# Kernel tuning notes

Hardware: AMD Instinct MI355X
Metric: run time of the kernel (lower is better)

## Reference

```python
import jax, jax.numpy as jnp
import numpy as np
from jax import lax

B, T, CIN, H, W = 2, 6, 1, 256, 256
COUT = 64
L = 13
H2, W2 = H // 2, W // 2


def conv2d(x, w, b, stride=1, pad=0):
    y = lax.conv_general_dilated(x, w, (stride, stride), [(pad, pad), (pad, pad)],
                                 dimension_numbers=('NCHW', 'OIHW', 'NCHW'))
    return y + b[None, :, None, None]


def leaky(x):
    return jnp.where(x >= 0, x, 0.2 * x)


def bilinear_sample(img, sx, sy):
    # img [B,C,H,W]; sx,sy [B,L,H,W] pixel coords; zero padding (grid_sample align_corners=True)
    Bc, C, Hh, Ww = img.shape
    x0 = jnp.floor(sx); y0 = jnp.floor(sy)
    x1 = x0 + 1.0; y1 = y0 + 1.0
    wx1 = sx - x0; wx0 = 1.0 - wx1
    wy1 = sy - y0; wy0 = 1.0 - wy1
    img_flat = img.reshape(Bc, C, Hh * Ww)

    def gather(xi, yi):
        valid = (xi >= 0) & (xi <= Ww - 1) & (yi >= 0) & (yi <= Hh - 1)
        xc = jnp.clip(xi, 0, Ww - 1).astype(jnp.int32)
        yc = jnp.clip(yi, 0, Hh - 1).astype(jnp.int32)
        idx = (yc * Ww + xc).reshape(Bc, 1, -1)
        g = jnp.take_along_axis(img_flat, idx, axis=2).reshape(Bc, C, *xi.shape[1:])
        return g * valid[:, None].astype(img.dtype)  # [B,C,L,H,W]

    return (gather(x0, y0) * (wx0 * wy0)[:, None]
            + gather(x1, y0) * (wx1 * wy0)[:, None]
            + gather(x0, y1) * (wx0 * wy1)[:, None]
            + gather(x1, y1) * (wx1 * wy1)[:, None])


def setup_inputs() -> dict:
    key = jax.random.key(0)
    ks = jax.random.split(key, 14)
    s = 0.05
    return {
        'x': jax.random.normal(ks[0], (B, T, CIN, H, W), jnp.float32),
        'w_stem': jax.random.normal(ks[1], (COUT * T, CIN * T, 3, 3), jnp.float32) * s,
        'b_stem': jnp.zeros((COUT * T,), jnp.float32),
        'w_i2h': jax.random.normal(ks[2], (3 * COUT, COUT, 3, 3), jnp.float32) * s,
        'b_i2h': jnp.zeros((3 * COUT,), jnp.float32),
        'w_i2f': jax.random.normal(ks[3], (32, COUT, 5, 5), jnp.float32) * s,
        'b_i2f': jnp.zeros((32,), jnp.float32),
        'w_h2f': jax.random.normal(ks[4], (32, COUT, 5, 5), jnp.float32) * s,
        'b_h2f': jnp.zeros((32,), jnp.float32),
        'w_flow': jax.random.normal(ks[5], (L * 2, 32, 5, 5), jnp.float32) * s,
        'b_flow': jnp.zeros((L * 2,), jnp.float32),
        'w_ret': jax.random.normal(ks[6], (3 * COUT, L * COUT, 1, 1), jnp.float32) * s,
        'b_ret': jnp.zeros((3 * COUT,), jnp.float32),
    }


def reference(x, w_stem, b_stem, w_i2h, b_i2h, w_i2f, b_i2f, w_h2f, b_h2f,
              w_flow, b_flow, w_ret, b_ret):
    Bq, Tq, Cq, Hq, Wq = x.shape
    h2, w2 = Hq // 2, Wq // 2
    # stem: fold T into channels, strided conv + leaky relu
    xs = x.reshape(Bq, Tq * Cq, Hq, Wq)
    ys = leaky(conv2d(xs, w_stem, b_stem, stride=2, pad=1))
    ys = ys.reshape(Bq, Tq, COUT, h2, w2)
    seq = jnp.transpose(ys, (1, 0, 2, 3, 4))  # [T,B,C,h,w]

    gy, gx = jnp.meshgrid(jnp.arange(h2, dtype=jnp.float32),
                          jnp.arange(w2, dtype=jnp.float32), indexing='ij')

    def step(hprev, xt):
        i2h = conv2d(xt, w_i2h, b_i2h, pad=1)  # [B,3C,h,w]
        f1 = leaky(conv2d(xt, w_i2f, b_i2f, pad=2) + conv2d(hprev, w_h2f, b_h2f, pad=2))
        flows = conv2d(f1, w_flow, b_flow, pad=2).reshape(Bq, L, 2, h2, w2)
        u, v = flows[:, :, 0], flows[:, :, 1]
        # wrap(h, -flow): sample at grid - flow
        sx = gx[None, None] - u
        sy = gy[None, None] - v
        warped = bilinear_sample(hprev, sx, sy)  # [B,C,L,h,w]
        warped = jnp.transpose(warped, (0, 2, 1, 3, 4)).reshape(Bq, L * COUT, h2, w2)
        h2h = conv2d(warped, w_ret, b_ret)  # 1x1 conv
        ir, iu, im = jnp.split(i2h, 3, axis=1)
        hr, hu, hm = jnp.split(h2h, 3, axis=1)
        r = jax.nn.sigmoid(ir + hr)
        z = jax.nn.sigmoid(iu + hu)
        m = leaky(im + r * hm)
        hnext = z * hprev + (1.0 - z) * m
        return hnext, hnext

    h0 = jnp.zeros((Bq, COUT, h2, w2), x.dtype)
    _, outs = lax.scan(step, h0, seq)  # [T,B,C,h,w]
    return jnp.transpose(outs, (1, 0, 2, 3, 4))
```

## Files before the change

### kernel.cpp

```cpp
#include <hip/hip_runtime.h>
#include <cstddef>

#define NPIX 16384
#define T_ 6

typedef __attribute__((ext_vector_type(8))) short bf16x8;
typedef __attribute__((ext_vector_type(4))) float f32x4;

__device__ __forceinline__ float leakyf(float x){ return x >= 0.f ? x : 0.2f*x; }
__device__ __forceinline__ float sigmf(float x){ return 1.f/(1.f+__expf(-x)); }
__device__ __forceinline__ short f2bf(float f){
    unsigned u = __float_as_uint(f);
    u += 0x7fffu + ((u>>16)&1u);
    return (short)(u>>16);
}
__device__ __forceinline__ float bf2f(short s){
    return __uint_as_float(((unsigned)(unsigned short)s)<<16);
}
__device__ __forceinline__ f32x4 MFMA(bf16x8 a, bf16x8 b, f32x4 c){
    return __builtin_amdgcn_mfma_f32_16x16x32_bf16(a, b, c, 0, 0, 0);
}

__global__ __launch_bounds__(256) void prep_w(const float* __restrict__ wi2h,
        const float* __restrict__ wf1i, const float* __restrict__ wf1h,
        const float* __restrict__ wfl, const float* __restrict__ wrt,
        const float* __restrict__ wst, short* __restrict__ dst){
    int idx = blockIdx.x*256 + threadIdx.x;
    float v;
    if(idx < 110592){
        int kk = idx/12288, r = idx%12288, oc = r>>6, ic = r&63;
        v = wi2h[((size_t)(oc*64+ic))*9 + kk];
    } else if(idx < 212992){
        int j = idx-110592; int tap = j>>11, r = j&2047, oc = r>>6, ic = r&63;
        int inp = tap/25, q = tap%25;
        const float* s = inp ? wf1h : wf1i;
        v = s[((size_t)(oc*64+ic))*25 + q];
    } else if(idx < 238592){
        int j = idx-212992; int q = j>>10, r = j&1023, oc = r>>5, ic = r&31;
        v = (oc < 26) ? wfl[((size_t)(oc*32+ic))*25 + q] : 0.f;
    } else if(idx < 398336){
        int j = idx-238592; int s_ = j/6144, r = j%6144, oc = r>>5, c = r&31;
        v = wrt[(size_t)oc*832 + s_*32 + c];
    } else {
        int j = idx-398336; int oc = j>>6, k = j&63;
        if(k < 54){ int ic = k/9, kk = k%9; v = wst[((size_t)(oc*6+ic))*9 + kk]; }
        else v = 0.f;
    }
    dst[idx] = f2bf(v);
}

__global__ __launch_bounds__(256) void stem_mfma(const float* __restrict__ x,
        const short* __restrict__ wS, const float* __restrict__ bias, short* __restrict__ ys_cl){
    __shared__ float xh[6*17*18];
    int bx = blockIdx.x;
    int ohalf = bx & 1, tile = (bx>>1) & 255, b = bx>>9;
    int ty0 = (tile>>4)*8, tx0 = (tile&15)*8;
    int tid = threadIdx.x, wid = tid>>6, lane = tid&63, lr = lane&15, lg = lane>>4;
    int iy0 = ty0*2-1, ix0 = tx0*2-1;
    for(int i=tid; i<1734; i+=256){
        int ic = i/289, r = i%289, hy = r/17, hx = r%17;
        int iy = iy0+hy, ix = ix0+hx;
        float v = 0.f;
        if((unsigned)iy<256u && (unsigned)ix<256u) v = x[((size_t)b*6+ic)*65536 + iy*256 + ix];
        xh[(ic*17+hy)*18+hx] = v;
    }
    __syncthreads();
    int pxl = wid*16 + lr;
    int ry = (pxl>>3)*2, rx = (pxl&7)*2;
    bf16x8 a[2];
    #pragma unroll
    for(int cg=0; cg<2; ++cg){
        #pragma unroll
        for(int e=0; e<8; ++e){
            int k = cg*32 + lg*8 + e;
            float v = 0.f;
            if(k < 54){
                int ic = k/9, t9 = k%9, ky = t9/3, kx = t9%3;
                v = xh[(ic*17 + ry+ky)*18 + rx+kx];
            }
            a[cg][e] = f2bf(v);
        }
    }
    short* yb = ys_cl + (size_t)b*NPIX*384;
    #pragma unroll
    for(int nj=0; nj<12; ++nj){
        int oc = (ohalf*12 + nj)*16 + lr;
        f32x4 acc = {};
        #pragma unroll
        for(int cg=0; cg<2; ++cg){
            bf16x8 bb = *(const bf16x8*)&wS[(size_t)oc*64 + cg*32 + lg*8];
            acc = MFMA(a[cg], bb, acc);
        }
        float bvs = bias[oc];
        #pragma unroll
        for(int r=0; r<4; ++r){
            int pxr = wid*16 + lg*4 + r;
            int pix = (ty0 + (pxr>>3))*128 + tx0 + (pxr&7);
            yb[(size_t)pix*384 + oc] = f2bf(leakyf(acc[r]+bvs));
        }
    }
}

__global__ __launch_bounds__(512) void ih_if_mfma(const short* __restrict__ ys_cl,
        const short* __restrict__ wI, const float* __restrict__ bI,
        const short* __restrict__ wF,
        float* __restrict__ i2h_all, float* __restrict__ f1i_all){
    __shared__ short xt[432*72];
    int bx = blockIdx.x;
    int tile = bx & 63; int r_ = bx >> 6; int t = r_ % 6; int b = r_ / 6;
    int ty0 = (tile>>2)*8, tx0 = (tile&3)*32;
    int tid = threadIdx.x, wid = tid>>6, lane = tid&63, lr = lane&15, lg = lane>>4;
    int mw = wid>>2, nw = wid&3;
    const short* xb = ys_cl + (size_t)b*NPIX*384 + t*64;
    for(int i=tid; i<3456; i+=512){
        int pix = i>>3, c8 = i&7;
        int hy = pix/36, hx = pix - hy*36;
        int py = ty0 - 2 + hy, px = tx0 - 2 + hx;
        bf16x8 v = {};
        if((unsigned)py < 128u && (unsigned)px < 128u)
            v = *(const bf16x8*)&xb[((size_t)py*128 + px)*384 + c8*8];
        *(bf16x8*)&xt[pix*72 + c8*8] = v;
    }
    __syncthreads();
    f32x4 accI[4][2][3] = {};
    for(int kk=0; kk<9; ++kk){
        int ky = kk/3, kx = kk - ky*3;
        #pragma unroll
        for(int cg=0; cg<2; ++cg){
            bf16x8 bv[3];
            #pragma unroll
            for(int ni=0; ni<3; ++ni)
                bv[ni] = *(const bf16x8*)&wI[((size_t)kk*192 + nw*48 + ni*16 + lr)*64 + cg*32 + lg*8];
            #pragma unroll
            for(int ri=0; ri<4; ++ri){
                int r2 = mw*4 + ri;
                bf16x8 av[2];
                #pragma unroll
                for(int mi=0; mi<2; ++mi){
                    int hp = (r2 + ky + 1)*36 + mi*16 + lr + kx + 1;
                    av[mi] = *(const bf16x8*)&xt[hp*72 + cg*32 + lg*8];
                }
                #pragma unroll
                for(int mi=0; mi<2; ++mi)
                  #pragma unroll
                  for(int ni=0; ni<3; ++ni)
                    accI[ri][mi][ni] = MFMA(av[mi], bv[ni], accI[ri][mi][ni]);
            }
        }
    }
    float* oI = i2h_all + ((size_t)t*2 + b)*192*NPIX;
    #pragma unroll
    for(int ri=0; ri<4; ++ri){
        int py = ty0 + mw*4 + ri;
        #pragma unroll
        for(int mi=0; mi<2; ++mi){
            int px = tx0 + mi*16 + lg*4;
            #pragma unroll
            for(int ni=0; ni<3; ++ni){
                int oc = nw*48 + ni*16 + lr;
                float bvs = bI[oc];
                f32x4 r = accI[ri][mi][ni];
                f32x4 st; st[0]=r[0]+bvs; st[1]=r[1]+bvs; st[2]=r[2]+bvs; st[3]=r[3]+bvs;
                *(f32x4*)&oI[(size_t)oc*NPIX + py*128 + px] = st;
            }
        }
    }
    f32x4 accF[4] = {};
    int mif = nw>>1, jF = (nw&1)*16 + lr;
    for(int q=0; q<25; ++q){
        int ky = q/5, kx = q - ky*5;
        #pragma unroll
        for(int cg=0; cg<2; ++cg){
            bf16x8 bb = *(const bf16x8*)&wF[((size_t)q*32 + (nw&1)*16 + lr)*64 + cg*32 + lg*8];
            #pragma unroll
            for(int ri=0; ri<4; ++ri){
                int hp = (mw*4 + ri + ky)*36 + mif*16 + lr + kx;
                bf16x8 av = *(const bf16x8*)&xt[hp*72 + cg*32 + lg*8];
                accF[ri] = MFMA(av, bb, accF[ri]);
            }
        }
    }
    float* oF = f1i_all + ((size_t)t*2 + b)*32*NPIX;
    #pragma unroll
    for(int ri=0; ri<4; ++ri){
        int py = ty0 + mw*4 + ri;
        int px = tx0 + mif*16 + lg*4;
        *(f32x4*)&oF[(size_t)jF*NPIX + py*128 + px] = accF[ri];
    }
}

__global__ __launch_bounds__(256) void f1h_mfma(const short* __restrict__ h_cl,
        const short* __restrict__ wF, const float* __restrict__ f1i_all, int t,
        const float* __restrict__ bi, const float* __restrict__ bh,
        short* __restrict__ f1_cl){
    __shared__ short xt[144*72];
    int bx = blockIdx.x;
    int tile = bx & 255, b = bx>>8;
    int ty0 = (tile>>4)*8, tx0 = (tile&15)*8;
    int tid = threadIdx.x, wid = tid>>6, lane = tid&63, lr = lane&15, lg = lane>>4;
    int mw = wid>>1, nw = wid&1;
    const short* xb = h_cl + (size_t)b*NPIX*64;
    for(int i=tid; i<1152; i+=256){
        int pix = i>>3, c8 = i&7;
        int hy = pix/12, hx = pix - hy*12;
        int py = ty0 - 2 + hy, px = tx0 - 2 + hx;
        bf16x8 v = {};
        if((unsigned)py < 128u && (unsigned)px < 128u)
            v = *(const bf16x8*)&xb[((size_t)py*128 + px)*64 + c8*8];
        *(bf16x8*)&xt[pix*72 + c8*8] = v;
    }
    __syncthreads();
    f32x4 acc[2] = {};
    for(int q=0; q<25; ++q){
        int ky = q/5, kx = q - ky*5;
        #pragma unroll
        for(int cg=0; cg<2; ++cg){
            bf16x8 av[2];
            #pragma unroll
            for(int mi=0; mi<2; ++mi){
                int m = mw*32 + mi*16 + lr;
                int hp = ((m>>3)+ky)*12 + (m&7)+kx;
                av[mi] = *(const bf16x8*)&xt[hp*72 + cg*32 + lg*8];
            }
            bf16x8 bb = *(const bf16x8*)&wF[((size_t)(25+q)*32 + nw*16 + lr)*64 + cg*32 + lg*8];
            #pragma unroll
            for(int mi=0; mi<2; ++mi) acc[mi] = MFMA(av[mi], bb, acc[mi]);
        }
    }
    int j = nw*16 + lr;
    float bvs = bi[j] + bh[j];
    const float* pF = f1i_all + ((size_t)t*2 + b)*32*NPIX;
    __syncthreads();
    #pragma unroll
    for(int mi=0; mi<2; ++mi){
        int m0 = mw*32 + mi*16 + lg*4;
        int py = ty0 + (m0>>3), px = tx0 + (m0&7);
        f32x4 p = *(const f32x4*)&pF[(size_t)j*NPIX + py*128 + px];
        #pragma unroll
        for(int r=0; r<4; ++r) xt[(m0+r)*40 + j] = f2bf(leakyf(acc[mi][r] + p[r] + bvs));
    }
    __syncthreads();
    {
        int px = tid>>2, c8 = tid&3;
        int pix = (ty0 + (px>>3))*128 + tx0 + (px&7);
        *(bf16x8*)&f1_cl[((size_t)b*NPIX + pix)*32 + c8*8] = *(const bf16x8*)&xt[px*40 + c8*8];
    }
}

__global__ __launch_bounds__(256) void flow_mfma(const short* __restrict__ f1_cl,
        const short* __restrict__ wA, const float* __restrict__ bias, float* __restrict__ flows){
    __shared__ short xt[144*40];
    int bx = blockIdx.x;
    int tile = bx & 255, b = bx>>8;
    int ty0 = (tile>>4)*8, tx0 = (tile&15)*8;
    int tid = threadIdx.x, wid = tid>>6, lane = tid&63, lr = lane&15, lg = lane>>4;
    int mw = wid>>1, nw = wid&1;
    f32x4 acc[2] = {};
    const short* xb = f1_cl + (size_t)b*NPIX*32;
    for(int i=tid; i<576; i+=256){
        int pix = i>>2, c8 = i&3;
        int hy = pix/12, hx = pix - hy*12;
        int py = ty0 - 2 + hy, px = tx0 - 2 + hx;
        bf16x8 v = {};
        if((unsigned)py < 128u && (unsigned)px < 128u)
            v = *(const bf16x8*)&xb[((size_t)py*128 + px)*32 + c8*8];
        *(bf16x8*)&xt[pix*40 + c8*8] = v;
    }
    __syncthreads();
    for(int ky=0; ky<5; ++ky){
        #pragma unroll
        for(int kx=0; kx<5; ++kx){
            bf16x8 av[2];
            #pragma unroll
            for(int mi=0; mi<2; ++mi){
                int m = mw*32 + mi*16 + lr;
                int hp = ((m>>3)+ky)*12 + (m&7) + kx;
                av[mi] = *(const bf16x8*)&xt[hp*40 + lg*8];
            }
            bf16x8 bb = *(const bf16x8*)&wA[((size_t)((ky*5+kx)*32) + nw*16 + lr)*32 + lg*8];
            #pragma unroll
            for(int mi=0; mi<2; ++mi) acc[mi] = MFMA(av[mi], bb, acc[mi]);
        }
    }
    int j = nw*16 + lr;
    if(j < 26){
        float bvs = bias[j];
        #pragma unroll
        for(int mi=0; mi<2; ++mi){
            int m0 = mw*32 + mi*16 + lg*4;
            int py = ty0 + (m0>>3), px = tx0 + (m0&7);
            f32x4 r = acc[mi];
            f32x4 st; st[0]=r[0]+bvs; st[1]=r[1]+bvs; st[2]=r[2]+bvs; st[3]=r[3]+bvs;
            *(f32x4*)&flows[((size_t)b*26 + j)*NPIX + py*128 + px] = st;
        }
    }
}

__device__ __forceinline__ void calc_corners(const float* __restrict__ s_sx,
        const float* __restrict__ s_sy, int l, int mypx,
        int& i00, int& i10, int& i01, int& i11,
        float& w00, float& w10, float& w01, float& w11){
    float sx = s_sx[l*64+mypx], sy = s_sy[l*64+mypx];
    float x0f = floorf(sx), y0f = floorf(sy);
    int x0 = (int)x0f, y0 = (int)y0f;
    float wx1 = sx-x0f, wy1 = sy-y0f, wx0 = 1.f-wx1, wy0 = 1.f-wy1;
    bool vx0 = (unsigned)x0<128u, vx1 = (unsigned)(x0+1)<128u;
    bool vy0 = (unsigned)y0<128u, vy1 = (unsigned)(y0+1)<128u;
    w00 = (vx0&&vy0)? wx0*wy0 : 0.f;
    w10 = (vx1&&vy0)? wx1*wy0 : 0.f;
    w01 = (vx0&&vy1)? wx0*wy1 : 0.f;
    w11 = (vx1&&vy1)? wx1*wy1 : 0.f;
    int xc0 = max(0,min(127,x0)), xc1 = max(0,min(127,x0+1));
    int yc0 = max(0,min(127,y0)), yc1 = max(0,min(127,y0+1));
    i00 = yc0*128+xc0; i10 = yc0*128+xc1; i01 = yc1*128+xc0; i11 = yc1*128+xc1;
}

__global__ __launch_bounds__(256) void warpret_mfma(
        const float* __restrict__ hprev_f32, int hstride,
        const short* __restrict__ h_in,
        const float* __restrict__ flows,
        const short* __restrict__ wret, const float* __restrict__ b_ret,
        const float* __restrict__ ib_f32, float* __restrict__ out,
        short* __restrict__ h_out, int t){
    __shared__ float s_sx[832], s_sy[832];
    __shared__ short At[2][64*40];
    __shared__ short Bt[2][192*40];
    int bx = blockIdx.x;
    int half = bx & 1, row = (bx>>1) & 127, b = bx >> 8;
    int pxbase = half*64;
    int tid = threadIdx.x, wid = tid>>6, lane = tid&63, lr = lane&15, lg = lane>>4;
    const short* hc = h_in + (size_t)b*NPIX*64;
    f32x4 acc[12] = {};
    for(int i=tid; i<832; i+=256){
        int l = i>>6, px = i&63;
        float u = flows[((size_t)b*26 + 2*l)*NPIX + row*128 + pxbase + px];
        float v = flows[((size_t)b*26 + 2*l+1)*NPIX + row*128 + pxbase + px];
        s_sx[i] = (float)(pxbase+px) - u;
        s_sy[i] = (float)row - v;
    }
    __syncthreads();

    int spx = tid & 63;
    int sch = tid >> 6;
    int brow = tid >> 2, bc4 = tid & 3;

    int i00,i10,i01,i11; float w00,w10,w01,w11;
    calc_corners(s_sx, s_sy, 0, spx, i00,i10,i01,i11, w00,w10,w01,w11);
    {
        int cb = sch*8;
        bf16x8 a00 = *(const bf16x8*)&hc[(size_t)i00*64 + cb];
        bf16x8 a10 = *(const bf16x8*)&hc[(size_t)i10*64 + cb];
        bf16x8 a01 = *(const bf16x8*)&hc[(size_t)i01*64 + cb];
        bf16x8 a11 = *(const bf16x8*)&hc[(size_t)i11*64 + cb];
        bf16x8 av;
        #pragma unroll
        for(int e=0; e<8; ++e)
            av[e] = f2bf(bf2f(a00[e])*w00 + bf2f(a10[e])*w10 +
                         bf2f(a01[e])*w01 + bf2f(a11[e])*w11);
        *(bf16x8*)&At[0][spx*40 + sch*8] = av;
        #pragma unroll
        for(int k=0; k<3; ++k)
            *(bf16x8*)&Bt[0][(brow + k*64)*40 + bc4*8] =
                *(const bf16x8*)&wret[((size_t)0*192 + brow + k*64)*32 + bc4*8];
    }
    __syncthreads();

    for(int s=0; s<26; ++s){
        int cur = s & 1, nxt = cur ^ 1;
        bf16x8 p00,p10,p01,p11, q0,q1,q2;
        if(s < 25){
            int sp = s+1, sl = sp>>1, scg = sp&1;
            if(scg == 0)
                calc_corners(s_sx, s_sy, sl, spx, i00,i10,i01,i11, w00,w10,w01,w11);
            int cb = scg*32 + sch*8;
            p00 = *(const bf16x8*)&hc[(size_t)i00*64 + cb];
            p10 = *(const bf16x8*)&hc[(size_t)i10*64 + cb];
            p01 = *(const bf16x8*)&hc[(size_t)i01*64 + cb];
            p11 = *(const bf16x8*)&hc[(size_t)i11*64 + cb];
            q0 = *(const bf16x8*)&wret[((size_t)sp*192 + brow      )*32 + bc4*8];
            q1 = *(const bf16x8*)&wret[((size_t)sp*192 + brow +  64)*32 + bc4*8];
            q2 = *(const bf16x8*)&wret[((size_t)sp*192 + brow + 128)*32 + bc4*8];
        }
        {
            bf16x8 a = *(const bf16x8*)&At[cur][(wid*16 + lr)*40 + lg*8];
            #pragma unroll
            for(int ni=0; ni<12; ++ni){
                bf16x8 bb = *(const bf16x8*)&Bt[cur][(ni*16 + lr)*40 + lg*8];
                acc[ni] = MFMA(a, bb, acc[ni]);
            }
        }
        if(s < 25){
            bf16x8 av;
            #pragma unroll
            for(int e=0; e<8; ++e)
                av[e] = f2bf(bf2f(p00[e])*w00 + bf2f(p10[e])*w10 +
                             bf2f(p01[e])*w01 + bf2f(p11[e])*w11);
            *(bf16x8*)&At[nxt][spx*40 + sch*8] = av;
            *(bf16x8*)&Bt[nxt][(brow      )*40 + bc4*8] = q0;
            *(bf16x8*)&Bt[nxt][(brow +  64)*40 + bc4*8] = q1;
            *(bf16x8*)&Bt[nxt][(brow + 128)*40 + bc4*8] = q2;
        }
        __syncthreads();
    }

    short* Ht = &Bt[0][0];
    const float* ib  = ib_f32 + (size_t)b*192*NPIX + row*128 + pxbase;
    const float* hbf = hprev_f32 + (size_t)b*hstride + row*128 + pxbase;
    float* ob = out + (((size_t)b*T_ + t)*64)*NPIX + row*128 + pxbase;
    int px4 = wid*16 + lg*4;
    #pragma unroll
    for(int ni=0; ni<4; ++ni){
        int oc = ni*16 + lr;
        f32x4 ir = *(const f32x4*)&ib[(size_t)oc*NPIX + px4];
        f32x4 iu = *(const f32x4*)&ib[(size_t)(64+oc)*NPIX + px4];
        f32x4 im = *(const f32x4*)&ib[(size_t)(128+oc)*NPIX + px4];
        f32x4 hp = *(const f32x4*)&hbf[(size_t)oc*NPIX + px4];
        float br = b_ret[oc], bu = b_ret[64+oc], bm = b_ret[128+oc];
        f32x4 st;
        #pragma unroll
        for(int r=0; r<4; ++r){
            float hr = acc[ni][r] + br;
            float hu = acc[ni+4][r] + bu;
            float hm = acc[ni+8][r] + bm;
            float rg = sigmf(ir[r] + hr);
            float zg = sigmf(iu[r] + hu);
            float mg = leakyf(im[r] + rg*hm);
            st[r] = zg*hp[r] + (1.f-zg)*mg;
        }
        *(f32x4*)&ob[(size_t)oc*NPIX + px4] = st;
        #pragma unroll
        for(int r=0; r<4; ++r) Ht[(px4+r)*72 + oc] = f2bf(st[r]);
    }
    __syncthreads();
    short* ho = h_out + ((size_t)b*NPIX + row*128 + pxbase)*64;
    for(int i=tid; i<512; i+=256){
        int px = i>>3, c8 = i&7;
        *(bf16x8*)&ho[(size_t)px*64 + c8*8] = *(const bf16x8*)&Ht[px*72 + c8*8];
    }
}

extern "C" void kernel_launch(void* const* d_in, const int* in_sizes, int n_in,
                              void* d_out, int out_size, void* d_ws, size_t ws_size,
                              hipStream_t stream) {
    const float* x      = (const float*)d_in[0];
    const float* w_stem = (const float*)d_in[1];
    const float* b_stem = (const float*)d_in[2];
    const float* w_i2h  = (const float*)d_in[3];
    const float* b_i2h  = (const float*)d_in[4];
    const float* w_i2f  = (const float*)d_in[5];
    const float* b_i2f  = (const float*)d_in[6];
    const float* w_h2f  = (const float*)d_in[7];
    const float* b_h2f  = (const float*)d_in[8];
    const float* w_flow = (const float*)d_in[9];
    const float* b_flow = (const float*)d_in[10];
    const float* w_ret  = (const float*)d_in[11];
    const float* b_ret  = (const float*)d_in[12];
    float* out = (float*)d_out;

    char* w = (char*)d_ws;
    float* h0_f32  = (float*)w;  w += (size_t)2*64*NPIX*4;
    float* i2h_all = (float*)w;  w += (size_t)6*2*192*NPIX*4;
    float* f1i_all = (float*)w;  w += (size_t)6*2*32*NPIX*4;
    float* flows   = (float*)w;  w += (size_t)2*26*NPIX*4;
    short* ys_cl   = (short*)w;  w += (size_t)2*NPIX*384*2;
    short* h_clA   = (short*)w;  w += (size_t)2*NPIX*64*2;
    short* h_clB   = (short*)w;  w += (size_t)2*NPIX*64*2;
    short* f1_cl   = (short*)w;  w += (size_t)2*NPIX*32*2;
    short* wAbase  = (short*)w;
    short* wA_i2h  = wAbase;
    short* wA_f1   = wAbase + 110592;
    short* wA_flow = wAbase + 212992;
    short* wA_ret  = wAbase + 238592;
    short* wA_stem = wAbase + 398336;

    prep_w<<<1652, 256, 0, stream>>>(w_i2h, w_i2f, w_h2f, w_flow, w_ret, w_stem, wAbase);
    hipMemsetAsync(h0_f32, 0, (size_t)2*64*NPIX*4, stream);
    hipMemsetAsync(h_clA, 0, (size_t)2*NPIX*64*2, stream);

    stem_mfma<<<1024, 256, 0, stream>>>(x, wA_stem, b_stem, ys_cl);
    ih_if_mfma<<<768, 512, 0, stream>>>(ys_cl, wA_i2h, b_i2h, wA_f1, i2h_all, f1i_all);

    for (int t = 0; t < T_; ++t) {
        const float* hprev = (t == 0) ? h0_f32 : out + (size_t)(t - 1) * 64 * NPIX;
        int hstride = (t == 0) ? 64 * NPIX : T_ * 64 * NPIX;
        short* h_in  = (t & 1) ? h_clB : h_clA;
        short* h_nxt = (t & 1) ? h_clA : h_clB;
        f1h_mfma<<<512, 256, 0, stream>>>(h_in, wA_f1, f1i_all, t, b_i2f, b_h2f, f1_cl);
        flow_mfma<<<512, 256, 0, stream>>>(f1_cl, wA_flow, b_flow, flows);
        warpret_mfma<<<512, 256, 0, stream>>>(hprev, hstride, h_in, flows,
                                              wA_ret, b_ret,
                                              i2h_all + ((size_t)t*2)*192*NPIX,
                                              out, h_nxt, t);
    }
}
```

Before: 510.7 us.

## Split warp-retrieve kernel into producer and consumer wavefronts

```diff
diff --git a/kernel.cpp b/kernel.cpp
--- a/kernel.cpp
+++ b/kernel.cpp
@@ -315,7 +315,7 @@
     i00 = yc0*128+xc0; i10 = yc0*128+xc1; i01 = yc1*128+xc0; i11 = yc1*128+xc1;
 }
 
-__global__ __launch_bounds__(256) void warpret_mfma(
+__global__ __launch_bounds__(512,2) void warpret_mfma(
         const float* __restrict__ hprev_f32, int hstride,
         const short* __restrict__ h_in,
         const float* __restrict__ flows,
@@ -329,9 +329,11 @@
     int half = bx & 1, row = (bx>>1) & 127, b = bx >> 8;
     int pxbase = half*64;
     int tid = threadIdx.x, wid = tid>>6, lane = tid&63, lr = lane&15, lg = lane>>4;
+    bool producer = tid >= 256;
+    int stid = tid & 255;
     const short* hc = h_in + (size_t)b*NPIX*64;
     f32x4 acc[12] = {};
-    for(int i=tid; i<832; i+=256){
+    for(int i=tid; i<832; i+=512){
         int l = i>>6, px = i&63;
         float u = flows[((size_t)b*26 + 2*l)*NPIX + row*128 + pxbase + px];
         float v = flows[((size_t)b*26 + 2*l+1)*NPIX + row*128 + pxbase + px];
@@ -340,13 +342,13 @@
     }
     __syncthreads();
 
-    int spx = tid & 63;
-    int sch = tid >> 6;
-    int brow = tid >> 2, bc4 = tid & 3;
-
-    int i00,i10,i01,i11; float w00,w10,w01,w11;
-    calc_corners(s_sx, s_sy, 0, spx, i00,i10,i01,i11, w00,w10,w01,w11);
-    {
+    int spx = stid & 63;
+    int sch = stid >> 6;
+    int brow = stid >> 2, bc4 = stid & 3;
+
+    int i00=0,i10=0,i01=0,i11=0; float w00=0,w10=0,w01=0,w11=0;
+    if(producer){
+        calc_corners(s_sx, s_sy, 0, spx, i00,i10,i01,i11, w00,w10,w01,w11);
         int cb = sch*8;
         bf16x8 a00 = *(const bf16x8*)&hc[(size_t)i00*64 + cb];
         bf16x8 a10 = *(const bf16x8*)&hc[(size_t)i10*64 + cb];
@@ -367,21 +369,30 @@
 
     for(int s=0; s<26; ++s){
         int cur = s & 1, nxt = cur ^ 1;
-        bf16x8 p00,p10,p01,p11, q0,q1,q2;
-        if(s < 25){
-            int sp = s+1, sl = sp>>1, scg = sp&1;
-            if(scg == 0)
-                calc_corners(s_sx, s_sy, sl, spx, i00,i10,i01,i11, w00,w10,w01,w11);
-            int cb = scg*32 + sch*8;
-            p00 = *(const bf16x8*)&hc[(size_t)i00*64 + cb];
-            p10 = *(const bf16x8*)&hc[(size_t)i10*64 + cb];
-            p01 = *(const bf16x8*)&hc[(size_t)i01*64 + cb];
-            p11 = *(const bf16x8*)&hc[(size_t)i11*64 + cb];
-            q0 = *(const bf16x8*)&wret[((size_t)sp*192 + brow      )*32 + bc4*8];
-            q1 = *(const bf16x8*)&wret[((size_t)sp*192 + brow +  64)*32 + bc4*8];
-            q2 = *(const bf16x8*)&wret[((size_t)sp*192 + brow + 128)*32 + bc4*8];
-        }
-        {
+        if(producer){
+            if(s < 25){
+                int sp = s+1, sl = sp>>1, scg = sp&1;
+                if(scg == 0)
+                    calc_corners(s_sx, s_sy, sl, spx, i00,i10,i01,i11, w00,w10,w01,w11);
+                int cb = scg*32 + sch*8;
+                bf16x8 p00 = *(const bf16x8*)&hc[(size_t)i00*64 + cb];
+                bf16x8 p10 = *(const bf16x8*)&hc[(size_t)i10*64 + cb];
+                bf16x8 p01 = *(const bf16x8*)&hc[(size_t)i01*64 + cb];
+                bf16x8 p11 = *(const bf16x8*)&hc[(size_t)i11*64 + cb];
+                bf16x8 q0 = *(const bf16x8*)&wret[((size_t)sp*192 + brow      )*32 + bc4*8];
+                bf16x8 q1 = *(const bf16x8*)&wret[((size_t)sp*192 + brow +  64)*32 + bc4*8];
+                bf16x8 q2 = *(const bf16x8*)&wret[((size_t)sp*192 + brow + 128)*32 + bc4*8];
+                bf16x8 av;
+                #pragma unroll
+                for(int e=0; e<8; ++e)
+                    av[e] = f2bf(bf2f(p00[e])*w00 + bf2f(p10[e])*w10 +
+                                 bf2f(p01[e])*w01 + bf2f(p11[e])*w11);
+                *(bf16x8*)&At[nxt][spx*40 + sch*8] = av;
+                *(bf16x8*)&Bt[nxt][(brow      )*40 + bc4*8] = q0;
+                *(bf16x8*)&Bt[nxt][(brow +  64)*40 + bc4*8] = q1;
+                *(bf16x8*)&Bt[nxt][(brow + 128)*40 + bc4*8] = q2;
+            }
+        } else {
             bf16x8 a = *(const bf16x8*)&At[cur][(wid*16 + lr)*40 + lg*8];
             #pragma unroll
             for(int ni=0; ni<12; ++ni){
@@ -389,52 +400,43 @@
                 acc[ni] = MFMA(a, bb, acc[ni]);
             }
         }
-        if(s < 25){
-            bf16x8 av;
-            #pragma unroll
-            for(int e=0; e<8; ++e)
-                av[e] = f2bf(bf2f(p00[e])*w00 + bf2f(p10[e])*w10 +
-                             bf2f(p01[e])*w01 + bf2f(p11[e])*w11);
-            *(bf16x8*)&At[nxt][spx*40 + sch*8] = av;
-            *(bf16x8*)&Bt[nxt][(brow      )*40 + bc4*8] = q0;
-            *(bf16x8*)&Bt[nxt][(brow +  64)*40 + bc4*8] = q1;
-            *(bf16x8*)&Bt[nxt][(brow + 128)*40 + bc4*8] = q2;
-        }
         __syncthreads();
     }
 
     short* Ht = &Bt[0][0];
-    const float* ib  = ib_f32 + (size_t)b*192*NPIX + row*128 + pxbase;
-    const float* hbf = hprev_f32 + (size_t)b*hstride + row*128 + pxbase;
-    float* ob = out + (((size_t)b*T_ + t)*64)*NPIX + row*128 + pxbase;
-    int px4 = wid*16 + lg*4;
-    #pragma unroll
-    for(int ni=0; ni<4; ++ni){
-        int oc = ni*16 + lr;
-        f32x4 ir = *(const f32x4*)&ib[(size_t)oc*NPIX + px4];
-        f32x4 iu = *(const f32x4*)&ib[(size_t)(64+oc)*NPIX + px4];
-        f32x4 im = *(const f32x4*)&ib[(size_t)(128+oc)*NPIX + px4];
-        f32x4 hp = *(const f32x4*)&hbf[(size_t)oc*NPIX + px4];
-        float br = b_ret[oc], bu = b_ret[64+oc], bm = b_ret[128+oc];
-        f32x4 st;
-        #pragma unroll
-        for(int r=0; r<4; ++r){
-            float hr = acc[ni][r] + br;
-            float hu = acc[ni+4][r] + bu;
-            float hm = acc[ni+8][r] + bm;
-            float rg = sigmf(ir[r] + hr);
-            float zg = sigmf(iu[r] + hu);
-            float mg = leakyf(im[r] + rg*hm);
-            st[r] = zg*hp[r] + (1.f-zg)*mg;
-        }
-        *(f32x4*)&ob[(size_t)oc*NPIX + px4] = st;
-        #pragma unroll
-        for(int r=0; r<4; ++r) Ht[(px4+r)*72 + oc] = f2bf(st[r]);
-    }
-    __syncthreads();
-    short* ho = h_out + ((size_t)b*NPIX + row*128 + pxbase)*64;
-    for(int i=tid; i<512; i+=256){
-        int px = i>>3, c8 = i&7;
+    if(!producer){
+        const float* ib  = ib_f32 + (size_t)b*192*NPIX + row*128 + pxbase;
+        const float* hbf = hprev_f32 + (size_t)b*hstride + row*128 + pxbase;
+        float* ob = out + (((size_t)b*T_ + t)*64)*NPIX + row*128 + pxbase;
+        int px4 = wid*16 + lg*4;
+        #pragma unroll
+        for(int ni=0; ni<4; ++ni){
+            int oc = ni*16 + lr;
+            f32x4 ir = *(const f32x4*)&ib[(size_t)oc*NPIX + px4];
+            f32x4 iu = *(const f32x4*)&ib[(size_t)(64+oc)*NPIX + px4];
+            f32x4 im = *(const f32x4*)&ib[(size_t)(128+oc)*NPIX + px4];
+            f32x4 hp = *(const f32x4*)&hbf[(size_t)oc*NPIX + px4];
+            float br = b_ret[oc], bu = b_ret[64+oc], bm = b_ret[128+oc];
+            f32x4 st;
+            #pragma unroll
+            for(int r=0; r<4; ++r){
+                float hr = acc[ni][r] + br;
+                float hu = acc[ni+4][r] + bu;
+                float hm = acc[ni+8][r] + bm;
+                float rg = sigmf(ir[r] + hr);
+                float zg = sigmf(iu[r] + hu);
+                float mg = leakyf(im[r] + rg*hm);
+                st[r] = zg*hp[r] + (1.f-zg)*mg;
+            }
+            *(f32x4*)&ob[(size_t)oc*NPIX + px4] = st;
+            #pragma unroll
+            for(int r=0; r<4; ++r) Ht[(px4+r)*72 + oc] = f2bf(st[r]);
+        }
+    }
+    __syncthreads();
+    {
+        int px = tid>>3, c8 = tid&7;
+        short* ho = h_out + ((size_t)b*NPIX + row*128 + pxbase)*64;
         *(bf16x8*)&ho[(size_t)px*64 + c8*8] = *(const bf16x8*)&Ht[px*72 + c8*8];
     }
 }
@@ -487,7 +489,7 @@
         short* h_nxt = (t & 1) ? h_clA : h_clB;
         f1h_mfma<<<512, 256, 0, stream>>>(h_in, wA_f1, f1i_all, t, b_i2f, b_h2f, f1_cl);
         flow_mfma<<<512, 256, 0, stream>>>(f1_cl, wA_flow, b_flow, flows);
-        warpret_mfma<<<512, 256, 0, stream>>>(hprev, hstride, h_in, flows,
+        warpret_mfma<<<512, 512, 0, stream>>>(hprev, hstride, h_in, flows,
                                               wA_ret, b_ret,
                                               i2h_all + ((size_t)t*2)*192*NPIX,
                                               out, h_nxt, t);
```

Result: slower. 524.0 us (+2.6%).
